# Kernel tuning notes

Measured on AMD Instinct MI355X. Metric: run time of the kernel, lower is better.

## Reference

```python
import jax, jax.numpy as jnp
import numpy as np

DIM, H, HD, S, K = 2560, 40, 64, 64, 4  # dim, n_heads, head_dim, state_dim, conv kernel
EPS = 1e-5


def _layer_norm(x, g, b):
    m = jnp.mean(x, axis=-1, keepdims=True)
    v = jnp.mean((x - m) ** 2, axis=-1, keepdims=True)
    return (x - m) * jax.lax.rsqrt(v + EPS) * g + b


def setup_inputs() -> dict:
    key = jax.random.key(0)
    ks = jax.random.split(key, 10)
    w = lambda k, shape: jax.random.normal(k, shape, jnp.float32) * 0.02
    return {
        "x": jax.random.normal(ks[0], (2, 2048, DIM), jnp.float32),
        "W_r": w(ks[1], (DIM, DIM)),
        "W_k": w(ks[2], (DIM, DIM)),
        "W_v": w(ks[3], (DIM, DIM)),
        "W_g": w(ks[4], (DIM, DIM)),
        "W_xproj": w(ks[5], (H * 3 * S, DIM)),
        "W_dt": w(ks[6], (DIM, H * S)),
        "b_dt": jnp.ones((DIM,), jnp.float32),  # dt_proj bias init to 1.0
        "conv_w": w(ks[7], (DIM, 1, K)),  # depthwise conv (out=DIM, in/groups=1, k)
        "ln1_g": jnp.ones((DIM,), jnp.float32),
        "ln1_b": jnp.zeros((DIM,), jnp.float32),
        "ln2_g": jnp.ones((DIM,), jnp.float32),
        "ln2_b": jnp.zeros((DIM,), jnp.float32),
        "W_out": w(ks[8], (DIM, DIM)),
    }


def reference(x, W_r, W_k, W_v, W_g, W_xproj, W_dt, b_dt, conv_w,
              ln1_g, ln1_b, ln2_g, ln2_b, W_out):
    B, L, D = x.shape
    # causal depthwise conv: torch Conv1d(pad=3)[:, :L] == left-pad by K-1
    xc = jax.lax.conv_general_dilated(
        x.transpose(0, 2, 1), conv_w, window_strides=(1,), padding=[(K - 1, 0)],
        feature_group_count=D, dimension_numbers=("NCH", "OIH", "NCH"),
    ).transpose(0, 2, 1)
    x = _layer_norm(x + xc, ln1_g, ln1_b)

    proj = (x @ W_xproj.T).reshape(B, L, H, 3 * S)
    dt_raw, B_vec, C_vec = jnp.split(proj, 3, axis=-1)  # each (B,L,H,S)
    dt = jax.nn.softplus(dt_raw.reshape(B, L, H * S) @ W_dt.T + b_dt)
    w = jnp.exp(-dt).reshape(B, L, H, S)

    r = jax.nn.sigmoid(x @ W_r.T).reshape(B, L, H, HD)
    k = (x @ W_k.T).reshape(B, L, H, HD)
    v = (x @ W_v.T).reshape(B, L, H, HD)
    g = jax.nn.sigmoid(x @ W_g.T).reshape(B, L, H, HD)
    kv = k * v  # (B,L,H,HD)

    def step(state, inp):
        w_t, B_t, C_t, kv_t, r_t, g_t = inp
        # state: (B,H,S,HD); decay per state row, rank-1 B ⊗ (k*v) update
        state = w_t[..., None] * state + B_t[..., None] * kv_t[:, :, None, :]
        y = jnp.einsum("bhsd,bhs->bhd", state, C_t)
        return state, r_t * y * g_t

    seq = tuple(jnp.moveaxis(a, 1, 0) for a in (w, B_vec, C_vec, kv, r, g))
    state0 = jnp.zeros((B, H, S, HD), x.dtype)
    final_state, outs = jax.lax.scan(step, state0, seq)  # outs: (L,B,H,HD)
    out = jnp.moveaxis(outs, 0, 1).reshape(B, L, D)
    out = _layer_norm(x + out @ W_out.T, ln2_g, ln2_b)
    return out, final_state
```

## Files before the change

kernel.cpp:

```cpp
#include <hip/hip_runtime.h>
#include <cstddef>
#include <cstdint>

#define DIM 2560
#define NH 40
#define HDD 64
#define SD 64
#define KC 4
#define BB 2
#define LL 2048
#define MTOT (BB*LL)
#define NPROJ (NH*3*SD)
#define NC 16
#define CH (LL/NC)
#define BH (BB*NH)

typedef unsigned short u16;
typedef __attribute__((ext_vector_type(8))) short bf16x8;
typedef __attribute__((ext_vector_type(4))) float f32x4;

__device__ inline float bf2f(u16 u) { return __uint_as_float(((unsigned)u) << 16); }
__device__ inline float bflo(unsigned u) { return __uint_as_float(u << 16); }
__device__ inline float bfhi(unsigned u) { return __uint_as_float(u & 0xffff0000u); }
__device__ inline u16 f2bf(float f) {
  unsigned x = __float_as_uint(f);
  unsigned r = (x + 0x7fffu + ((x >> 16) & 1u)) >> 16;
  return (u16)r;
}

__device__ inline void gload16(const void* g, void* lds) {
  __builtin_amdgcn_global_load_lds(
      (const __attribute__((address_space(1))) void*)g,
      (__attribute__((address_space(3))) void*)(uint32_t)(size_t)lds,
      16, 0, 0);
}

__global__ __launch_bounds__(256) void cvt_kernel(
    const float* __restrict__ src, u16* __restrict__ dst, int n4) {
  int i = blockIdx.x * 256 + threadIdx.x;
  int stride = gridDim.x * 256;
  for (; i < n4; i += stride) {
    float4 v = *(const float4*)(src + (size_t)i * 4);
    ushort4 o;
    o.x = f2bf(v.x); o.y = f2bf(v.y); o.z = f2bf(v.z); o.w = f2bf(v.w);
    *(ushort4*)(dst + (size_t)i * 4) = o;
  }
}

__global__ __launch_bounds__(256) void fill_kernel(float* p, int n, float v) {
  int i = blockIdx.x * 256 + threadIdx.x;
  if (i < n) p[i] = v;
}

__device__ inline void block_reduce2(float& sum, float& sq, float* red) {
  #pragma unroll
  for (int off = 32; off; off >>= 1) {
    sum += __shfl_down(sum, off, 64);
    sq  += __shfl_down(sq,  off, 64);
  }
  int wid = threadIdx.x >> 6, lane = threadIdx.x & 63;
  if (lane == 0) { red[wid*2] = sum; red[wid*2+1] = sq; }
  __syncthreads();
  sum = red[0] + red[2] + red[4] + red[6];
  sq  = red[1] + red[3] + red[5] + red[7];
}

__global__ __launch_bounds__(256) void conv_ln1_kernel(
    const float* __restrict__ x, const float* __restrict__ cw,
    const float* __restrict__ g1, const float* __restrict__ b1,
    u16* __restrict__ x1) {
  __shared__ float red[8];
  int bl = blockIdx.x;
  int l  = bl & (LL - 1);
  int t  = threadIdx.x;
  const float* xr = x + (size_t)bl * DIM;
  float vals[10];
  float sum = 0.f, sq = 0.f;
  #pragma unroll
  for (int i = 0; i < 10; ++i) {
    int d = t + 256 * i;
    float acc = xr[d];
    #pragma unroll
    for (int j = 0; j < KC; ++j) {
      int ll = l - (KC - 1) + j;
      if (ll >= 0) acc += x[(size_t)(bl - l + ll) * DIM + d] * cw[d * KC + j];
    }
    vals[i] = acc; sum += acc; sq += acc * acc;
  }
  block_reduce2(sum, sq, red);
  float mean = sum * (1.f / DIM);
  float var  = sq * (1.f / DIM) - mean * mean;
  float rstd = rsqrtf(var + 1e-5f);
  u16* orow = x1 + (size_t)bl * DIM;
  #pragma unroll
  for (int i = 0; i < 10; ++i) {
    int d = t + 256 * i;
    orow[d] = f2bf((vals[i] - mean) * rstd * g1[d] + b1[d]);
  }
}

__global__ __launch_bounds__(256) void ln2_kernel(
    const u16* __restrict__ x1, const u16* __restrict__ y2,
    const float* __restrict__ g2, const float* __restrict__ b2,
    float* __restrict__ out) {
  __shared__ float red[8];
  int bl = blockIdx.x;
  int t  = threadIdx.x;
  const u16* ar = x1 + (size_t)bl * DIM;
  const u16* br = y2 + (size_t)bl * DIM;
  float vals[10];
  float sum = 0.f, sq = 0.f;
  #pragma unroll
  for (int i = 0; i < 10; ++i) {
    int d = t + 256 * i;
    float v = bf2f(ar[d]) + bf2f(br[d]);
    vals[i] = v; sum += v; sq += v * v;
  }
  block_reduce2(sum, sq, red);
  float mean = sum * (1.f / DIM);
  float var  = sq * (1.f / DIM) - mean * mean;
  float rstd = rsqrtf(var + 1e-5f);
  float* orow = out + (size_t)bl * DIM;
  #pragma unroll
  for (int i = 0; i < 10; ++i) {
    int d = t + 256 * i;
    orow[d] = (vals[i] - mean) * rstd * g2[d] + b2[d];
  }
}

template<int EPI, bool REMAP>
__global__ __launch_bounds__(256) void gemm_mfma(
    const u16* __restrict__ A, int lda,
    const u16* __restrict__ Wb,
    const float* __restrict__ bias,
    u16* __restrict__ C1, int ldc,
    int K) {
  __shared__ u16 As[128 * 32];
  __shared__ u16 Bs[128 * 32];
  int t = threadIdx.x;
  int w = t >> 6, l = t & 63;
  int wr = w >> 1, wc = w & 1;
  int m0 = blockIdx.y * 128;
  int n0 = blockIdx.x * 128;

  f32x4 acc[4][4];
  #pragma unroll
  for (int i = 0; i < 4; ++i)
    #pragma unroll
    for (int j = 0; j < 4; ++j)
      acc[i][j] = (f32x4){0.f, 0.f, 0.f, 0.f};

  int srow = 32 * w + (l >> 2);
  int scol = (l & 3) * 8;
  const u16* gA = A  + (size_t)(m0 + srow) * lda + scol;
  const u16* gB = Wb + (size_t)(n0 + srow) * K   + scol;
  u16* ldsA = As + (32 * w) * 32;
  u16* ldsB = Bs + (32 * w) * 32;

  int fr = l & 15;
  int kc = (l >> 4) * 8;
  const u16* rA = As + (size_t)(wr * 64 + fr) * 32 + kc;
  const u16* rB = Bs + (size_t)(wc * 64 + fr) * 32 + kc;

  for (int k0 = 0; k0 < K; k0 += 32) {
    gload16(gA + k0, ldsA);
    gload16(gA + (size_t)16 * lda + k0, ldsA + 16 * 32);
    gload16(gB + k0, ldsB);
    gload16(gB + (size_t)16 * K + k0, ldsB + 16 * 32);
    __syncthreads();
    bf16x8 a[4], b[4];
    #pragma unroll
    for (int i = 0; i < 4; ++i) a[i] = *(const bf16x8*)(rA + i * 16 * 32);
    #pragma unroll
    for (int j = 0; j < 4; ++j) b[j] = *(const bf16x8*)(rB + j * 16 * 32);
    #pragma unroll
    for (int i = 0; i < 4; ++i)
      #pragma unroll
      for (int j = 0; j < 4; ++j)
        acc[i][j] = __builtin_amdgcn_mfma_f32_16x16x32_bf16(a[i], b[j], acc[i][j], 0, 0, 0);
    __syncthreads();
  }

  int crow = (l >> 4) * 4;
  int ccol = l & 15;
  #pragma unroll
  for (int j = 0; j < 4; ++j) {
    int col = n0 + wc * 64 + j * 16 + ccol;
    int colr = col;
    if (REMAP) {
      int h = col / 192, r3 = col % 192;
      colr = (r3 / 64) * 2560 + h * 64 + (r3 & 63);
    }
    float bv = (EPI == 2) ? bias[col] : 0.f;
    #pragma unroll
    for (int i = 0; i < 4; ++i) {
      #pragma unroll
      for (int q = 0; q < 4; ++q) {
        int row = m0 + wr * 64 + i * 16 + crow + q;
        float v = acc[i][j][q];
        if constexpr (EPI == 2) v = 1.f / (1.f + expf(v + bv));
        C1[(size_t)row * ldc + colr] = f2bf(v);
      }
    }
  }
}

__global__ __launch_bounds__(256) void gemm_big4(
    const u16* __restrict__ A,
    const u16* __restrict__ W0, const u16* __restrict__ W1,
    const u16* __restrict__ W2, const u16* __restrict__ W3,
    u16* __restrict__ C0, u16* __restrict__ C1b,
    u16* __restrict__ C2, u16* __restrict__ C3,
    int K) {
  __shared__ u16 As[128 * 32];
  __shared__ u16 Bs[128 * 32];
  int t = threadIdx.x;
  int w = t >> 6, l = t & 63;
  int wr = w >> 1, wc = w & 1;
  int m0 = blockIdx.y * 128;
  int n0g = blockIdx.x * 128;
  int which = n0g / 2560;
  int n0 = n0g - which * 2560;
  const u16* Wsel = (which == 0) ? W0 : (which == 1) ? W1 : (which == 2) ? W2 : W3;
  u16* Csel = (which == 0) ? C0 : (which == 1) ? C1b : (which == 2) ? C2 : C3;
  bool sig = (which < 2);

  f32x4 acc[4][4];
  #pragma unroll
  for (int i = 0; i < 4; ++i)
    #pragma unroll
    for (int j = 0; j < 4; ++j)
      acc[i][j] = (f32x4){0.f, 0.f, 0.f, 0.f};

  int srow = 32 * w + (l >> 2);
  int scol = (l & 3) * 8;
  const u16* gA = A    + (size_t)(m0 + srow) * K + scol;
  const u16* gB = Wsel + (size_t)(n0 + srow) * K + scol;
  u16* ldsA = As + (32 * w) * 32;
  u16* ldsB = Bs + (32 * w) * 32;

  int fr = l & 15;
  int kc = (l >> 4) * 8;
  const u16* rA = As + (size_t)(wr * 64 + fr) * 32 + kc;
  const u16* rB = Bs + (size_t)(wc * 64 + fr) * 32 + kc;

  for (int k0 = 0; k0 < K; k0 += 32) {
    gload16(gA + k0, ldsA);
    gload16(gA + (size_t)16 * K + k0, ldsA + 16 * 32);
    gload16(gB + k0, ldsB);
    gload16(gB + (size_t)16 * K + k0, ldsB + 16 * 32);
    __syncthreads();
    bf16x8 a[4], b[4];
    #pragma unroll
    for (int i = 0; i < 4; ++i) a[i] = *(const bf16x8*)(rA + i * 16 * 32);
    #pragma unroll
    for (int j = 0; j < 4; ++j) b[j] = *(const bf16x8*)(rB + j * 16 * 32);
    #pragma unroll
    for (int i = 0; i < 4; ++i)
      #pragma unroll
      for (int j = 0; j < 4; ++j)
        acc[i][j] = __builtin_amdgcn_mfma_f32_16x16x32_bf16(a[i], b[j], acc[i][j], 0, 0, 0);
    __syncthreads();
  }

  int crow = (l >> 4) * 4;
  int ccol = l & 15;
  #pragma unroll
  for (int j = 0; j < 4; ++j) {
    int col = n0 + wc * 64 + j * 16 + ccol;
    #pragma unroll
    for (int i = 0; i < 4; ++i) {
      #pragma unroll
      for (int q = 0; q < 4; ++q) {
        int row = m0 + wr * 64 + i * 16 + crow + q;
        float v = acc[i][j][q];
        if (sig) v = 1.f / (1.f + expf(-v));
        Csel[(size_t)row * DIM + col] = f2bf(v);
      }
    }
  }
}

__global__ __launch_bounds__(128) void scan_local_kernel(
    const u16* __restrict__ wdec, const u16* __restrict__ proj,
    const u16* __restrict__ kb, const u16* __restrict__ vb,
    u16* __restrict__ yout,
    float* __restrict__ Sbuf, float* __restrict__ Pbuf) {
  int bx = blockIdx.x;
  int bh = bx / NC, c = bx % NC;
  int b = bh / NH, h = bh % NH;
  int wv = threadIdx.x >> 6;
  int lane = threadIdx.x & 63;
  int sg = lane >> 3, dd = lane & 7;
  int s0 = sg * 8;
  int d0 = wv * 32 + dd * 4;
  int l0 = c * CH;

  const u16* fw = wdec + ((size_t)(b * LL + l0)) * DIM + h * 64 + s0;
  const u16* fB = proj + ((size_t)(b * LL + l0)) * NPROJ + 2560 + h * 64 + s0;
  const u16* fC = fB + 2560;
  const u16* fk = kb + ((size_t)(b * LL + l0)) * DIM + h * 64 + d0;
  const u16* fv = vb + ((size_t)(b * LL + l0)) * DIM + h * 64 + d0;
  u16* py = yout + ((size_t)(b * LL + l0)) * NPROJ + h * 64 + d0;

  float st[8][4];
  float pc[8];
  #pragma unroll
  for (int i = 0; i < 8; ++i) {
    pc[i] = 1.f;
    #pragma unroll
    for (int j = 0; j < 4; ++j) st[i][j] = 0.f;
  }

#define P1_DECL(n) uint4 wS##n, BS##n, CS##n; uint2 kS##n, vS##n
#define P1_LOAD(n) do { \
    wS##n = *(const uint4*)fw; BS##n = *(const uint4*)fB; \
    CS##n = *(const uint4*)fC; kS##n = *(const uint2*)fk; \
    vS##n = *(const uint2*)fv; \
    fw += DIM; fB += NPROJ; fC += NPROJ; fk += DIM; fv += DIM; } while (0)
#define P1_PROC(n) do { \
    float wv8[8], Bv[8], Cv[8], kv4[4], pr[4]; \
    wv8[0]=bflo(wS##n.x); wv8[1]=bfhi(wS##n.x); wv8[2]=bflo(wS##n.y); wv8[3]=bfhi(wS##n.y); \
    wv8[4]=bflo(wS##n.z); wv8[5]=bfhi(wS##n.z); wv8[6]=bflo(wS##n.w); wv8[7]=bfhi(wS##n.w); \
    Bv[0]=bflo(BS##n.x); Bv[1]=bfhi(BS##n.x); Bv[2]=bflo(BS##n.y); Bv[3]=bfhi(BS##n.y); \
    Bv[4]=bflo(BS##n.z); Bv[5]=bfhi(BS##n.z); Bv[6]=bflo(BS##n.w); Bv[7]=bfhi(BS##n.w); \
    Cv[0]=bflo(CS##n.x); Cv[1]=bfhi(CS##n.x); Cv[2]=bflo(CS##n.y); Cv[3]=bfhi(CS##n.y); \
    Cv[4]=bflo(CS##n.z); Cv[5]=bfhi(CS##n.z); Cv[6]=bflo(CS##n.w); Cv[7]=bfhi(CS##n.w); \
    kv4[0]=bflo(kS##n.x)*bflo(vS##n.x); kv4[1]=bfhi(kS##n.x)*bfhi(vS##n.x); \
    kv4[2]=bflo(kS##n.y)*bflo(vS##n.y); kv4[3]=bfhi(kS##n.y)*bfhi(vS##n.y); \
    pr[0]=0.f; pr[1]=0.f; pr[2]=0.f; pr[3]=0.f; \
    _Pragma("unroll") \
    for (int i = 0; i < 8; ++i) { \
      pc[i] *= wv8[i]; \
      _Pragma("unroll") \
      for (int j = 0; j < 4; ++j) { \
        st[i][j] = fmaf(wv8[i], st[i][j], Bv[i] * kv4[j]); \
        pr[j] = fmaf(st[i][j], Cv[i], pr[j]); } } \
    _Pragma("unroll") \
    for (int j = 0; j < 4; ++j) { \
      pr[j] += __shfl_xor(pr[j], 8, 64); \
      pr[j] += __shfl_xor(pr[j], 16, 64); \
      pr[j] += __shfl_xor(pr[j], 32, 64); } \
    if (lane < 8) { \
      uint2 ov; \
      ov.x = (unsigned)f2bf(pr[0]) | ((unsigned)f2bf(pr[1]) << 16); \
      ov.y = (unsigned)f2bf(pr[2]) | ((unsigned)f2bf(pr[3]) << 16); \
      *(uint2*)py = ov; } \
    py += NPROJ; } while (0)

  P1_DECL(0); P1_DECL(1); P1_DECL(2); P1_DECL(3);
  P1_LOAD(0); P1_LOAD(1); P1_LOAD(2); P1_LOAD(3);
  for (int l = 0; l < CH; l += 4) {
    P1_PROC(0); P1_LOAD(0);
    P1_PROC(1); P1_LOAD(1);
    P1_PROC(2); P1_LOAD(2);
    P1_PROC(3); P1_LOAD(3);
  }
#undef P1_DECL
#undef P1_LOAD
#undef P1_PROC

  float* Sp = Sbuf + (((size_t)c * BH + bh) * 64 + s0) * 64 + d0;
  #pragma unroll
  for (int i = 0; i < 8; ++i) {
    float4 v; v.x = st[i][0]; v.y = st[i][1]; v.z = st[i][2]; v.w = st[i][3];
    *(float4*)(Sp + (size_t)i * 64) = v;
  }
  if (wv == 0 && dd == 0) {
    #pragma unroll
    for (int i = 0; i < 8; ++i)
      Pbuf[((size_t)c * BH + bh) * 64 + s0 + i] = pc[i];
  }
}

__global__ __launch_bounds__(256) void scan_combine_kernel(
    float* __restrict__ Sbuf, const float* __restrict__ Pbuf,
    float* __restrict__ fstate) {
  int bh = blockIdx.x;
  int t = threadIdx.x;
  int s = t >> 2, j0 = (t & 3) * 16;
  float stin[16];
  #pragma unroll
  for (int k = 0; k < 16; ++k) stin[k] = 0.f;
  for (int c = 0; c < NC; ++c) {
    float* Sp = Sbuf + (((size_t)c * BH + bh) * 64 + s) * 64 + j0;
    float Pc = Pbuf[((size_t)c * BH + bh) * 64 + s];
    #pragma unroll
    for (int q = 0; q < 4; ++q) {
      float4 a = *(const float4*)(Sp + q * 4);
      float4 cur;
      cur.x = stin[q*4+0]; cur.y = stin[q*4+1];
      cur.z = stin[q*4+2]; cur.w = stin[q*4+3];
      *(float4*)(Sp + q * 4) = cur;
      stin[q*4+0] = a.x + Pc * stin[q*4+0];
      stin[q*4+1] = a.y + Pc * stin[q*4+1];
      stin[q*4+2] = a.z + Pc * stin[q*4+2];
      stin[q*4+3] = a.w + Pc * stin[q*4+3];
    }
  }
  float* fp = fstate + ((size_t)bh * 64 + s) * 64 + j0;
  #pragma unroll
  for (int q = 0; q < 4; ++q) {
    float4 v;
    v.x = stin[q*4+0]; v.y = stin[q*4+1];
    v.z = stin[q*4+2]; v.w = stin[q*4+3];
    *(float4*)(fp + q * 4) = v;
  }
}

__global__ __launch_bounds__(128) void scan_correct_kernel(
    const u16* __restrict__ wdec, const u16* __restrict__ proj,
    const u16* __restrict__ rb, const u16* __restrict__ gb,
    const float* __restrict__ Sbuf, u16* __restrict__ yio) {
  int bx = blockIdx.x;
  int bh = bx / NC, c = bx % NC;
  int b = bh / NH, h = bh % NH;
  int wv = threadIdx.x >> 6;
  int lane = threadIdx.x & 63;
  int sg = lane >> 3, dd = lane & 7;
  int s0 = sg * 8;
  int d0 = wv * 32 + dd * 4;
  int l0 = c * CH;

  const float* Sp = Sbuf + (((size_t)c * BH + bh) * 64 + s0) * 64 + d0;
  float stin[8][4];
  #pragma unroll
  for (int i = 0; i < 8; ++i) {
    float4 v = *(const float4*)(Sp + (size_t)i * 64);
    stin[i][0] = v.x; stin[i][1] = v.y; stin[i][2] = v.z; stin[i][3] = v.w;
  }

  const u16* fw = wdec + ((size_t)(b * LL + l0)) * DIM + h * 64 + s0;
  const u16* fC = proj + ((size_t)(b * LL + l0)) * NPROJ + 5120 + h * 64 + s0;
  const u16* fy = yio  + ((size_t)(b * LL + l0)) * NPROJ + h * 64 + d0;
  const u16* fr2 = rb + ((size_t)(b * LL + l0)) * DIM + h * 64 + d0;
  const u16* fg2 = gb + ((size_t)(b * LL + l0)) * DIM + h * 64 + d0;
  u16* py = yio + ((size_t)(b * LL + l0)) * NPROJ + h * 64 + d0;

  float pc[8];
  #pragma unroll
  for (int i = 0; i < 8; ++i) pc[i] = 1.f;

#define P3_DECL(n) uint4 wT##n, CT##n; uint2 yT##n, rT##n, gT##n
#define P3_LOAD(n) do { \
    wT##n = *(const uint4*)fw; CT##n = *(const uint4*)fC; \
    yT##n = *(const uint2*)fy; rT##n = *(const uint2*)fr2; gT##n = *(const uint2*)fg2; \
    fw += DIM; fC += NPROJ; fy += NPROJ; fr2 += DIM; fg2 += DIM; } while (0)
#define P3_PROC(n) do { \
    float wv8[8], Cv[8], ac[8], pr[4]; \
    wv8[0]=bflo(wT##n.x); wv8[1]=bfhi(wT##n.x); wv8[2]=bflo(wT##n.y); wv8[3]=bfhi(wT##n.y); \
    wv8[4]=bflo(wT##n.z); wv8[5]=bfhi(wT##n.z); wv8[6]=bflo(wT##n.w); wv8[7]=bfhi(wT##n.w); \
    Cv[0]=bflo(CT##n.x); Cv[1]=bfhi(CT##n.x); Cv[2]=bflo(CT##n.y); Cv[3]=bfhi(CT##n.y); \
    Cv[4]=bflo(CT##n.z); Cv[5]=bfhi(CT##n.z); Cv[6]=bflo(CT##n.w); Cv[7]=bfhi(CT##n.w); \
    pr[0]=0.f; pr[1]=0.f; pr[2]=0.f; pr[3]=0.f; \
    _Pragma("unroll") \
    for (int i = 0; i < 8; ++i) { \
      pc[i] *= wv8[i]; ac[i] = pc[i] * Cv[i]; \
      _Pragma("unroll") \
      for (int j = 0; j < 4; ++j) pr[j] = fmaf(ac[i], stin[i][j], pr[j]); } \
    _Pragma("unroll") \
    for (int j = 0; j < 4; ++j) { \
      pr[j] += __shfl_xor(pr[j], 8, 64); \
      pr[j] += __shfl_xor(pr[j], 16, 64); \
      pr[j] += __shfl_xor(pr[j], 32, 64); } \
    if (lane < 8) { \
      float y0 = (bflo(yT##n.x) + pr[0]) * bflo(rT##n.x) * bflo(gT##n.x); \
      float y1 = (bfhi(yT##n.x) + pr[1]) * bfhi(rT##n.x) * bfhi(gT##n.x); \
      float y2 = (bflo(yT##n.y) + pr[2]) * bflo(rT##n.y) * bflo(gT##n.y); \
      float y3 = (bfhi(yT##n.y) + pr[3]) * bfhi(rT##n.y) * bfhi(gT##n.y); \
      uint2 ov; \
      ov.x = (unsigned)f2bf(y0) | ((unsigned)f2bf(y1) << 16); \
      ov.y = (unsigned)f2bf(y2) | ((unsigned)f2bf(y3) << 16); \
      *(uint2*)py = ov; } \
    py += NPROJ; } while (0)

  P3_DECL(0); P3_DECL(1); P3_DECL(2); P3_DECL(3);
  P3_LOAD(0); P3_LOAD(1); P3_LOAD(2); P3_LOAD(3);
  for (int l = 0; l < CH; l += 4) {
    P3_PROC(0); P3_LOAD(0);
    P3_PROC(1); P3_LOAD(1);
    P3_PROC(2); P3_LOAD(2);
    P3_PROC(3); P3_LOAD(3);
  }
#undef P3_DECL
#undef P3_LOAD
#undef P3_PROC
}

extern "C" void kernel_launch(void* const* d_in, const int* in_sizes, int n_in,
                              void* d_out, int out_size, void* d_ws, size_t ws_size,
                              hipStream_t stream) {
  const float* x    = (const float*)d_in[0];
  const float* W_r  = (const float*)d_in[1];
  const float* W_k  = (const float*)d_in[2];
  const float* W_v  = (const float*)d_in[3];
  const float* W_g  = (const float*)d_in[4];
  const float* W_xp = (const float*)d_in[5];
  const float* W_dt = (const float*)d_in[6];
  const float* b_dt = (const float*)d_in[7];
  const float* cw   = (const float*)d_in[8];
  const float* ln1g = (const float*)d_in[9];
  const float* ln1b = (const float*)d_in[10];
  const float* ln2g = (const float*)d_in[11];
  const float* ln2b = (const float*)d_in[12];
  const float* W_o  = (const float*)d_in[13];

  float* out    = (float*)d_out;
  float* fstate = out + (size_t)MTOT * DIM;

  const size_t nBL = (size_t)MTOT * DIM;
  const size_t nPJ = (size_t)MTOT * NPROJ;
  const size_t nWX = (size_t)NPROJ * DIM;
  const size_t nDD = (size_t)DIM * DIM;
  const size_t needed = (nBL * 5 + nPJ + nWX) * sizeof(u16);
  if (ws_size < needed) {
    fill_kernel<<<(out_size + 255) / 256, 256, 0, stream>>>(out, out_size, 1234.5f);
    return;
  }

  u16* wsp  = (u16*)d_ws;
  u16* x1   = wsp;
  u16* proj = x1 + nBL;
  u16* wdec = proj + nPJ;
  u16* rb   = wdec + nBL;
  u16* gb   = rb + nBL;
  u16* kvb  = gb + nBL;
  u16* wscr = kvb + nBL;
  float* Sbuf = (float*)wscr;
  float* Pbuf = Sbuf + (size_t)NC * BH * 64 * 64;

  u16* vscr = (u16*)d_out;
  u16* wvb  = vscr + nBL;

  const int nDD4 = (int)(nDD / 4);

  conv_ln1_kernel<<<MTOT, 256, 0, stream>>>(x, cw, ln1g, ln1b, x1);

  cvt_kernel<<<2048, 256, 0, stream>>>(W_xp, wscr, NPROJ * DIM / 4);
  gemm_mfma<0,true ><<<dim3(NPROJ/128, MTOT/128), 256, 0, stream>>>(x1, DIM, wscr, nullptr, proj, NPROJ, DIM);

  cvt_kernel<<<2048, 256, 0, stream>>>(W_dt, wscr, nDD4);
  gemm_mfma<2,false><<<dim3(DIM/128, MTOT/128), 256, 0, stream>>>(proj, NPROJ, wscr, b_dt, wdec, DIM, DIM);

  cvt_kernel<<<2048, 256, 0, stream>>>(W_r, wscr, nDD4);
  cvt_kernel<<<2048, 256, 0, stream>>>(W_g, wscr + nDD, nDD4);
  cvt_kernel<<<2048, 256, 0, stream>>>(W_k, wscr + 2 * nDD, nDD4);
  cvt_kernel<<<2048, 256, 0, stream>>>(W_v, wvb, nDD4);
  gemm_big4<<<dim3(4 * DIM / 128, MTOT / 128), 256, 0, stream>>>(
      x1, wscr, wscr + nDD, wscr + 2 * nDD, wvb, rb, gb, kvb, vscr, DIM);

  scan_local_kernel<<<BH * NC, 128, 0, stream>>>(wdec, proj, kvb, vscr, proj, Sbuf, Pbuf);
  scan_combine_kernel<<<BH, 256, 0, stream>>>(Sbuf, Pbuf, fstate);
  scan_correct_kernel<<<BH * NC, 128, 0, stream>>>(wdec, proj, rb, gb, Sbuf, proj);

  cvt_kernel<<<2048, 256, 0, stream>>>(W_o, wscr, nDD4);
  gemm_mfma<0,false><<<dim3(DIM/128, MTOT/128), 256, 0, stream>>>(proj, NPROJ, wscr, nullptr, wdec, DIM, DIM);

  ln2_kernel<<<MTOT, 256, 0, stream>>>(x1, wdec, ln2g, ln2b, out);
}
```

Baseline: 1.053 ms.

## Double-buffer LDS in MFMA GEMMs and merge four weight conversions

Both bf16 MFMA GEMM kernels now use two LDS buffers and issue async global-to-LDS loads two K-tiles ahead, using explicit vmcnt waits, s_barrier and raised wave priority around the MFMA block. The goal is to overlap global memory latency with matrix math instead of stalling on each tile. Separately, the four weight fp32-to-bf16 conversion launches are merged into one kernel to cut launch overhead. LDS use per block doubles, which may lower occupancy, and the hand-written waitcnt logic has to match the number of loads in flight exactly.

Measured after the change: 987.7 us. -6.2%, faster.

```diff
diff --git a/kernel.cpp b/kernel.cpp
--- a/kernel.cpp
+++ b/kernel.cpp
@@ -47,6 +47,24 @@
   }
 }
 
+struct Cvt4Args { const float* s0; const float* s1; const float* s2; const float* s3;
+                  u16* d0; u16* d1; u16* d2; u16* d3; };
+__global__ __launch_bounds__(256) void cvt4_kernel(Cvt4Args a, int n4each) {
+  int i = blockIdx.x * 256 + threadIdx.x;
+  int stride = gridDim.x * 256;
+  int total = 4 * n4each;
+  for (; i < total; i += stride) {
+    int which = i / n4each;
+    int loc = i - which * n4each;
+    const float* s = (which == 0) ? a.s0 : (which == 1) ? a.s1 : (which == 2) ? a.s2 : a.s3;
+    u16* d = (which == 0) ? a.d0 : (which == 1) ? a.d1 : (which == 2) ? a.d2 : a.d3;
+    float4 v = *(const float4*)(s + (size_t)loc * 4);
+    ushort4 o;
+    o.x = f2bf(v.x); o.y = f2bf(v.y); o.z = f2bf(v.z); o.w = f2bf(v.w);
+    *(ushort4*)(d + (size_t)loc * 4) = o;
+  }
+}
+
 __global__ __launch_bounds__(256) void fill_kernel(float* p, int n, float v) {
   int i = blockIdx.x * 256 + threadIdx.x;
   if (i < n) p[i] = v;
@@ -128,6 +146,37 @@
   }
 }
 
+#define GEMM_PIPE_LOOP(STAGEM) \
+  STAGEM(0, 0); \
+  STAGEM(1, 32); \
+  { \
+    int nt = K / 32; \
+    for (int tt = 0; tt < nt; ++tt) { \
+      if (tt == nt - 1) { asm volatile("s_waitcnt vmcnt(0)" ::: "memory"); } \
+      else              { asm volatile("s_waitcnt vmcnt(4)" ::: "memory"); } \
+      __builtin_amdgcn_sched_barrier(0); \
+      __builtin_amdgcn_s_barrier(); \
+      __builtin_amdgcn_sched_barrier(0); \
+      int buf = tt & 1; \
+      bf16x8 a[4], b[4]; \
+      _Pragma("unroll") \
+      for (int i = 0; i < 4; ++i) a[i] = *(const bf16x8*)(rA + buf * 4096 + i * 16 * 32); \
+      _Pragma("unroll") \
+      for (int j = 0; j < 4; ++j) b[j] = *(const bf16x8*)(rB + buf * 4096 + j * 16 * 32); \
+      __builtin_amdgcn_s_setprio(1); \
+      _Pragma("unroll") \
+      for (int i = 0; i < 4; ++i) \
+        _Pragma("unroll") \
+        for (int j = 0; j < 4; ++j) \
+          acc[i][j] = __builtin_amdgcn_mfma_f32_16x16x32_bf16(a[i], b[j], acc[i][j], 0, 0, 0); \
+      __builtin_amdgcn_s_setprio(0); \
+      __builtin_amdgcn_sched_barrier(0); \
+      __builtin_amdgcn_s_barrier(); \
+      __builtin_amdgcn_sched_barrier(0); \
+      if (tt + 2 < nt) { int k2 = (tt + 2) * 32; STAGEM(buf, k2); } \
+    } \
+  }
+
 template<int EPI, bool REMAP>
 __global__ __launch_bounds__(256) void gemm_mfma(
     const u16* __restrict__ A, int lda,
@@ -135,8 +184,8 @@
     const float* __restrict__ bias,
     u16* __restrict__ C1, int ldc,
     int K) {
-  __shared__ u16 As[128 * 32];
-  __shared__ u16 Bs[128 * 32];
+  __shared__ u16 As[2 * 128 * 32];
+  __shared__ u16 Bs[2 * 128 * 32];
   int t = threadIdx.x;
   int w = t >> 6, l = t & 63;
   int wr = w >> 1, wc = w & 1;
@@ -154,32 +203,21 @@
   int scol = (l & 3) * 8;
   const u16* gA = A  + (size_t)(m0 + srow) * lda + scol;
   const u16* gB = Wb + (size_t)(n0 + srow) * K   + scol;
-  u16* ldsA = As + (32 * w) * 32;
-  u16* ldsB = Bs + (32 * w) * 32;
+  int ldsOff = (32 * w) * 32;
 
   int fr = l & 15;
   int kc = (l >> 4) * 8;
   const u16* rA = As + (size_t)(wr * 64 + fr) * 32 + kc;
   const u16* rB = Bs + (size_t)(wc * 64 + fr) * 32 + kc;
 
-  for (int k0 = 0; k0 < K; k0 += 32) {
-    gload16(gA + k0, ldsA);
-    gload16(gA + (size_t)16 * lda + k0, ldsA + 16 * 32);
-    gload16(gB + k0, ldsB);
-    gload16(gB + (size_t)16 * K + k0, ldsB + 16 * 32);
-    __syncthreads();
-    bf16x8 a[4], b[4];
-    #pragma unroll
-    for (int i = 0; i < 4; ++i) a[i] = *(const bf16x8*)(rA + i * 16 * 32);
-    #pragma unroll
-    for (int j = 0; j < 4; ++j) b[j] = *(const bf16x8*)(rB + j * 16 * 32);
-    #pragma unroll
-    for (int i = 0; i < 4; ++i)
-      #pragma unroll
-      for (int j = 0; j < 4; ++j)
-        acc[i][j] = __builtin_amdgcn_mfma_f32_16x16x32_bf16(a[i], b[j], acc[i][j], 0, 0, 0);
-    __syncthreads();
-  }
+#define STAGE_S(buf, k0) do { \
+    gload16(gA + (k0), As + (buf) * 4096 + ldsOff); \
+    gload16(gA + (size_t)16 * lda + (k0), As + (buf) * 4096 + ldsOff + 16 * 32); \
+    gload16(gB + (k0), Bs + (buf) * 4096 + ldsOff); \
+    gload16(gB + (size_t)16 * K + (k0), Bs + (buf) * 4096 + ldsOff + 16 * 32); } while (0)
+
+  GEMM_PIPE_LOOP(STAGE_S)
+#undef STAGE_S
 
   int crow = (l >> 4) * 4;
   int ccol = l & 15;
@@ -212,8 +250,8 @@
     u16* __restrict__ C0, u16* __restrict__ C1b,
     u16* __restrict__ C2, u16* __restrict__ C3,
     int K) {
-  __shared__ u16 As[128 * 32];
-  __shared__ u16 Bs[128 * 32];
+  __shared__ u16 As[2 * 128 * 32];
+  __shared__ u16 Bs[2 * 128 * 32];
   int t = threadIdx.x;
   int w = t >> 6, l = t & 63;
   int wr = w >> 1, wc = w & 1;
@@ -236,32 +274,21 @@
   int scol = (l & 3) * 8;
   const u16* gA = A    + (size_t)(m0 + srow) * K + scol;
   const u16* gB = Wsel + (size_t)(n0 + srow) * K + scol;
-  u16* ldsA = As + (32 * w) * 32;
-  u16* ldsB = Bs + (32 * w) * 32;
+  int ldsOff = (32 * w) * 32;
 
   int fr = l & 15;
   int kc = (l >> 4) * 8;
   const u16* rA = As + (size_t)(wr * 64 + fr) * 32 + kc;
   const u16* rB = Bs + (size_t)(wc * 64 + fr) * 32 + kc;
 
-  for (int k0 = 0; k0 < K; k0 += 32) {
-    gload16(gA + k0, ldsA);
-    gload16(gA + (size_t)16 * K + k0, ldsA + 16 * 32);
-    gload16(gB + k0, ldsB);
-    gload16(gB + (size_t)16 * K + k0, ldsB + 16 * 32);
-    __syncthreads();
-    bf16x8 a[4], b[4];
-    #pragma unroll
-    for (int i = 0; i < 4; ++i) a[i] = *(const bf16x8*)(rA + i * 16 * 32);
-    #pragma unroll
-    for (int j = 0; j < 4; ++j) b[j] = *(const bf16x8*)(rB + j * 16 * 32);
-    #pragma unroll
-    for (int i = 0; i < 4; ++i)
-      #pragma unroll
-      for (int j = 0; j < 4; ++j)
-        acc[i][j] = __builtin_amdgcn_mfma_f32_16x16x32_bf16(a[i], b[j], acc[i][j], 0, 0, 0);
-    __syncthreads();
-  }
+#define STAGE_B(buf, k0) do { \
+    gload16(gA + (k0), As + (buf) * 4096 + ldsOff); \
+    gload16(gA + (size_t)16 * K + (k0), As + (buf) * 4096 + ldsOff + 16 * 32); \
+    gload16(gB + (k0), Bs + (buf) * 4096 + ldsOff); \
+    gload16(gB + (size_t)16 * K + (k0), Bs + (buf) * 4096 + ldsOff + 16 * 32); } while (0)
+
+  GEMM_PIPE_LOOP(STAGE_B)
+#undef STAGE_B
 
   int crow = (l >> 4) * 4;
   int ccol = l & 15;
@@ -542,10 +569,10 @@
   cvt_kernel<<<2048, 256, 0, stream>>>(W_dt, wscr, nDD4);
   gemm_mfma<2,false><<<dim3(DIM/128, MTOT/128), 256, 0, stream>>>(proj, NPROJ, wscr, b_dt, wdec, DIM, DIM);
 
-  cvt_kernel<<<2048, 256, 0, stream>>>(W_r, wscr, nDD4);
-  cvt_kernel<<<2048, 256, 0, stream>>>(W_g, wscr + nDD, nDD4);
-  cvt_kernel<<<2048, 256, 0, stream>>>(W_k, wscr + 2 * nDD, nDD4);
-  cvt_kernel<<<2048, 256, 0, stream>>>(W_v, wvb, nDD4);
+  Cvt4Args ca;
+  ca.s0 = W_r; ca.s1 = W_g; ca.s2 = W_k; ca.s3 = W_v;
+  ca.d0 = wscr; ca.d1 = wscr + nDD; ca.d2 = wscr + 2 * nDD; ca.d3 = wvb;
+  cvt4_kernel<<<2048, 256, 0, stream>>>(ca, nDD4);
   gemm_big4<<<dim3(4 * DIM / 128, MTOT / 128), 256, 0, stream>>>(
       x1, wscr, wscr + nDD, wscr + 2 * nDD, wvb, rb, gb, kvb, vscr, DIM);
 
```
